# Kernel tuning notes

Hardware: AMD Instinct MI355X
Metric: run time of the kernel (lower is better)

Reference implementation:

```python
import jax, jax.numpy as jnp
import numpy as np
import math

H = 4            # cross_attn_heads
SPARSE_RATIO = 0.6
B, N, C = 128, 196, 768


def setup_inputs() -> dict:
    key = jax.random.key(0)
    ks = jax.random.split(key, 10)
    xav = (6.0 / (C + C)) ** 0.5  # xavier_uniform bound for square Linear
    inp = {
        "RGB_cash": jax.random.normal(ks[0], (B, N, C), jnp.float32),
        "NI_cash": jax.random.normal(ks[1], (B, N, C), jnp.float32),
        "TI_cash": jax.random.normal(ks[2], (B, N, C), jnp.float32),
        "RGB_global": jax.random.normal(ks[3], (B, C), jnp.float32),
        "NI_global": jax.random.normal(ks[4], (B, C), jnp.float32),
        "TI_global": jax.random.normal(ks[5], (B, C), jnp.float32),
        # 9 CrossModalAttention modules, stacked: q_proj / k_proj weights (out,in) and biases
        "q_w": jax.random.uniform(ks[6], (9, C, C), jnp.float32, -xav, xav),
        "q_b": jnp.zeros((9, C), jnp.float32),
        "k_w": jax.random.uniform(ks[7], (9, C, C), jnp.float32, -xav, xav),
        "k_b": jnp.zeros((9, C), jnp.float32),
        # 3 TokenSparse modal_weights, init torch.ones(3); small noise for non-degenerate softmax
        "modal_w": jnp.ones((3, 3), jnp.float32) + 0.01 * jax.random.normal(ks[8], (3, 3), jnp.float32),
    }
    return inp


def _cos_sim(patches, g):
    # patches (B,N,C), g (B,C) -> (B,N); F.normalize eps=1e-12
    pn = patches / jnp.maximum(jnp.linalg.norm(patches, axis=-1, keepdims=True), 1e-12)
    gn = g / jnp.maximum(jnp.linalg.norm(g, axis=-1, keepdims=True), 1e-12)
    return jnp.einsum("bnc,bc->bn", pn, gn)


def _cross_attn(patches, g, cos, qw, qb, kw, kb):
    # CrossModalAttention.forward: Q from global (1 token), K from patches, softmax over N
    b, n, c = patches.shape
    d = c // H
    q = (g @ qw.T + qb).reshape(b, H, d)              # (B,H,D)
    k = (patches @ kw.T + kb).reshape(b, n, H, d)     # (B,N,H,D)
    attn = jnp.einsum("bhd,bnhd->bhn", q, k) * (d ** -0.5)
    attn = jax.nn.softmax(attn, axis=-1)              # (B,H,N)
    return (attn * cos[:, None, :]).mean(axis=1)      # (B,N)


def _minmax(s):
    smin = s.min(axis=-1, keepdims=True)
    smax = s.max(axis=-1, keepdims=True)
    return (s - smin) / (smax - smin + 1e-8)


def _token_sparse(tokens, s_im, s_m2, s_m3, mw):
    b, n, c = tokens.shape
    w = jax.nn.softmax(mw)
    score = w[0] * _minmax(s_im) + w[1] * _minmax(s_m2) + w[2] * _minmax(s_m3)
    num_keep = max(1, math.ceil(n * SPARSE_RATIO))
    _, idx = jax.lax.top_k(score, num_keep)           # == descending sort, first num_keep
    mask = jnp.zeros((b, n), score.dtype).at[jnp.arange(b)[:, None], idx].set(1.0)
    return tokens * mask[..., None], mask


def reference(RGB_cash, NI_cash, TI_cash, RGB_global, NI_global, TI_global,
              q_w, q_b, k_w, k_b, modal_w):
    toks = [RGB_cash, NI_cash, TI_cash]
    glbs = [RGB_global, NI_global, TI_global]
    # module order: rgb_self, rgb_x_nir, rgb_x_tir, nir_self, nir_x_rgb, nir_x_tir,
    #               tir_self, tir_x_rgb, tir_x_nir
    order = [(0, 0), (0, 1), (0, 2), (1, 1), (1, 0), (1, 2), (2, 2), (2, 0), (2, 1)]
    scores = []
    for i, (pi, gi) in enumerate(order):
        cos = _cos_sim(toks[pi], glbs[gi])
        scores.append(_cross_attn(toks[pi], glbs[gi], cos, q_w[i], q_b[i], k_w[i], k_b[i]))
    out_rgb, m_rgb = _token_sparse(RGB_cash, scores[0], scores[1], scores[2], modal_w[0])
    out_nir, m_nir = _token_sparse(NI_cash, scores[3], scores[4], scores[5], modal_w[1])
    out_tir, m_tir = _token_sparse(TI_cash, scores[6], scores[7], scores[8], modal_w[2])
    return (out_rgb, out_nir, out_tir, m_rgb, m_nir, m_tir)
```

## Files before the change

### kernel.cpp

```cpp
#include <hip/hip_runtime.h>
#include <math.h>

#define BB   128
#define NN   196
#define CC   768
#define HH   4
#define DD   192
#define TOK_PER   19267584
#define NROWS_ALL 75264
#define F4_ALL    14450688
#define NUM_KEEP  118

#define OFF_QPART 0
#define SZ_QPART  (2*9*128*768)
#define OFF_VV    (OFF_QPART + SZ_QPART)
#define SZ_VV     (9*128*4*768)
#define OFF_BIAS  (OFF_VV + SZ_VV)
#define SZ_BIAS   (9*128*4)
#define OFF_GN    (OFF_BIAS + SZ_BIAS)
#define SZ_GN     (3*128*768)
#define OFF_LOG   (OFF_GN + SZ_GN)
#define SZ_LOG    (9*128*4*196)
#define OFF_COS   (OFF_LOG + SZ_LOG)

__device__ __forceinline__ float4 f4fma(float s, float4 b, float4 a) {
  a.x = fmaf(s, b.x, a.x); a.y = fmaf(s, b.y, a.y);
  a.z = fmaf(s, b.z, a.z); a.w = fmaf(s, b.w, a.w);
  return a;
}

__global__ __launch_bounds__(256) void k_gnorm(const float* __restrict__ g0,
                                               const float* __restrict__ g1,
                                               const float* __restrict__ g2,
                                               float* __restrict__ gn) {
  int wid = (blockIdx.x * 256 + threadIdx.x) >> 6;
  int lane = threadIdx.x & 63;
  if (wid >= 384) return;
  int t = wid >> 7, b = wid & 127;
  const float* src = (t == 0) ? g0 : ((t == 1) ? g1 : g2);
  const float4* s4 = (const float4*)(src + (size_t)b * CC);
  float4 v0 = s4[lane], v1 = s4[lane + 64], v2 = s4[lane + 128];
  float ss = v0.x*v0.x + v0.y*v0.y + v0.z*v0.z + v0.w*v0.w
           + v1.x*v1.x + v1.y*v1.y + v1.z*v1.z + v1.w*v1.w
           + v2.x*v2.x + v2.y*v2.y + v2.z*v2.z + v2.w*v2.w;
  #pragma unroll
  for (int off = 32; off; off >>= 1) ss += __shfl_xor(ss, off);
  float inv = 1.0f / fmaxf(sqrtf(ss), 1e-12f);
  float4* d4 = (float4*)(gn + ((size_t)t * 128 + b) * CC);
  v0.x *= inv; v0.y *= inv; v0.z *= inv; v0.w *= inv;
  v1.x *= inv; v1.y *= inv; v1.z *= inv; v1.w *= inv;
  v2.x *= inv; v2.y *= inv; v2.z *= inv; v2.w *= inv;
  d4[lane] = v0; d4[lane + 64] = v1; d4[lane + 128] = v2;
}

__global__ __launch_bounds__(256) void k_qproj(const float* __restrict__ g0,
                                               const float* __restrict__ g1,
                                               const float* __restrict__ g2,
                                               const float* __restrict__ qw,
                                               float* __restrict__ qpart) {
  __shared__ __align__(16) float AsT[32 * 68];
  __shared__ __align__(16) float WsT[32 * 68];
  const int gtab[9] = {0, 1, 2, 1, 0, 2, 2, 0, 1};
  int i = blockIdx.y, z = blockIdx.z;
  int mt = blockIdx.x & 1, nt = blockIdx.x >> 1;
  int tid = threadIdx.x, tx = tid & 15, ty = tid >> 4;
  int gi = gtab[i];
  const float4* A4 = (const float4*)((gi == 0) ? g0 : ((gi == 1) ? g1 : g2));
  const float4* W4 = (const float4*)(qw + (size_t)i * CC * CC);
  float4 acc0 = {0,0,0,0}, acc1 = {0,0,0,0}, acc2 = {0,0,0,0}, acc3 = {0,0,0,0};
  int arow = mt * 64, wrow = nt * 64;
  int kb4 = z * 96;
  for (int kk = 0; kk < 12; kk++) {
    #pragma unroll
    for (int f = tid; f < 512; f += 256) {
      int r = f >> 3, k4 = f & 7;
      float4 va = A4[(size_t)(arow + r) * 192 + kb4 + kk * 8 + k4];
      float4 vw = W4[(size_t)(wrow + r) * 192 + kb4 + kk * 8 + k4];
      int kq = 4 * k4;
      AsT[(kq+0)*68 + r] = va.x; AsT[(kq+1)*68 + r] = va.y;
      AsT[(kq+2)*68 + r] = va.z; AsT[(kq+3)*68 + r] = va.w;
      WsT[(kq+0)*68 + r] = vw.x; WsT[(kq+1)*68 + r] = vw.y;
      WsT[(kq+2)*68 + r] = vw.z; WsT[(kq+3)*68 + r] = vw.w;
    }
    __syncthreads();
    #pragma unroll
    for (int k = 0; k < 32; k++) {
      float4 a = *(const float4*)&AsT[k * 68 + 4 * ty];
      float4 w = *(const float4*)&WsT[k * 68 + 4 * tx];
      acc0 = f4fma(a.x, w, acc0); acc1 = f4fma(a.y, w, acc1);
      acc2 = f4fma(a.z, w, acc2); acc3 = f4fma(a.w, w, acc3);
    }
    __syncthreads();
  }
  float* dst = qpart + (size_t)(z * 9 + i) * 128 * CC;
  int col = wrow + 4 * tx;
  int row = arow + 4 * ty;
  *(float4*)&dst[(size_t)(row + 0) * CC + col] = acc0;
  *(float4*)&dst[(size_t)(row + 1) * CC + col] = acc1;
  *(float4*)&dst[(size_t)(row + 2) * CC + col] = acc2;
  *(float4*)&dst[(size_t)(row + 3) * CC + col] = acc3;
}

__global__ __launch_bounds__(256) void k_vvproj(const float* __restrict__ qpart,
                                                const float* __restrict__ qb,
                                                const float* __restrict__ kw,
                                                float* __restrict__ vvout) {
  __shared__ __align__(16) float AsT[32 * 68];
  __shared__ __align__(16) float Bs[32 * 68];
  int ih = blockIdx.y; int i = ih >> 2, h = ih & 3;
  int mt = blockIdx.x & 1, nt = blockIdx.x >> 1;
  int tid = threadIdx.x, tx = tid & 15, ty = tid >> 4;
  const float4* qp0 = (const float4*)qpart + (size_t)i * 128 * 192;
  const float4* qp1 = (const float4*)qpart + (size_t)(9 + i) * 128 * 192;
  const float4* qb4 = (const float4*)qb + (size_t)i * 192;
  const float4* B4  = (const float4*)(kw + (size_t)i * CC * CC);
  float4 acc0 = {0,0,0,0}, acc1 = {0,0,0,0}, acc2 = {0,0,0,0}, acc3 = {0,0,0,0};
  int arow = mt * 64;
  int bcol4 = nt * 16;
  for (int kk = 0; kk < 6; kk++) {
    #pragma unroll
    for (int f = tid; f < 512; f += 256) {
      int r = f >> 3, k4 = f & 7;
      int colf4 = h * 48 + kk * 8 + k4;
      float4 va = qp0[(size_t)(arow + r) * 192 + colf4];
      float4 vb = qp1[(size_t)(arow + r) * 192 + colf4];
      float4 vq = qb4[colf4];
      va.x += vb.x + vq.x; va.y += vb.y + vq.y;
      va.z += vb.z + vq.z; va.w += vb.w + vq.w;
      int kq = 4 * k4;
      AsT[(kq+0)*68 + r] = va.x; AsT[(kq+1)*68 + r] = va.y;
      AsT[(kq+2)*68 + r] = va.z; AsT[(kq+3)*68 + r] = va.w;
      int rk = f >> 4, c4 = f & 15;
      float4 vB = B4[(size_t)(h * DD + kk * 32 + rk) * 192 + bcol4 + c4];
      *(float4*)&Bs[rk * 68 + 4 * c4] = vB;
    }
    __syncthreads();
    #pragma unroll
    for (int k = 0; k < 32; k++) {
      float4 a = *(const float4*)&AsT[k * 68 + 4 * ty];
      float4 bb = *(const float4*)&Bs[k * 68 + 4 * tx];
      acc0 = f4fma(a.x, bb, acc0); acc1 = f4fma(a.y, bb, acc1);
      acc2 = f4fma(a.z, bb, acc2); acc3 = f4fma(a.w, bb, acc3);
    }
    __syncthreads();
  }
  int col = nt * 64 + 4 * tx;
  int b0 = arow + 4 * ty;
  *(float4*)&vvout[((size_t)(i * 128 + b0 + 0) * 4 + h) * CC + col] = acc0;
  *(float4*)&vvout[((size_t)(i * 128 + b0 + 1) * 4 + h) * CC + col] = acc1;
  *(float4*)&vvout[((size_t)(i * 128 + b0 + 2) * 4 + h) * CC + col] = acc2;
  *(float4*)&vvout[((size_t)(i * 128 + b0 + 3) * 4 + h) * CC + col] = acc3;
}

__global__ __launch_bounds__(128) void k_bias(const float* __restrict__ qpart,
                                              const float* __restrict__ qb,
                                              const float* __restrict__ kb,
                                              float* __restrict__ bias) {
  int ih = blockIdx.x; int i = ih >> 2, h = ih & 3;
  int b = threadIdx.x;
  const float* q0  = qpart + ((size_t)i * 128 + b) * CC + h * DD;
  const float* q1  = qpart + ((size_t)(9 + i) * 128 + b) * CC + h * DD;
  const float* qbb = qb + (size_t)i * CC + h * DD;
  const float* kbb = kb + (size_t)i * CC + h * DD;
  float s = 0.f;
  for (int j = 0; j < DD; j++) s = fmaf(q0[j] + q1[j] + qbb[j], kbb[j], s);
  bias[((size_t)i * 128 + b) * 4 + h] = s;
}

__global__ __launch_bounds__(128) void k_dots(const float* __restrict__ rgb,
                                              const float* __restrict__ ni,
                                              const float* __restrict__ ti,
                                              const float* __restrict__ vv,
                                              const float* __restrict__ gn,
                                              const float* __restrict__ bias,
                                              float* __restrict__ logits,
                                              float* __restrict__ cosm) {
  __shared__ __align__(16) float V[15 * 768];
  int bid = blockIdx.x;
  int t = bid >> 8;
  int rem = bid & 255;
  int b = rem >> 1, half = rem & 1;
  const float* toks = (t == 0) ? rgb : ((t == 1) ? ni : ti);
  float4* V4 = (float4*)V;
  for (int f = threadIdx.x; f < 15 * 192; f += 128) {
    int v = f / 192, c4 = f - v * 192;
    const float4* src;
    if (v < 12) {
      int k = v >> 2, h = v & 3;
      src = (const float4*)(vv + (((size_t)(3 * t + k) * 128 + b) * 4 + h) * CC);
    } else {
      src = (const float4*)(gn + ((size_t)(v - 12) * 128 + b) * CC);
    }
    V4[f] = src[c4];
  }
  __syncthreads();
  int tid = threadIdx.x;
  if (tid >= 98) return;
  int n = half * 98 + tid;
  const float4* P4 = (const float4*)(toks + ((size_t)b * NN + n) * CC);
  float acc[16];
  #pragma unroll
  for (int v = 0; v < 16; v++) acc[v] = 0.f;
  #pragma unroll 2
  for (int c4 = 0; c4 < 192; c4++) {
    float4 p = P4[c4];
    #pragma unroll
    for (int v = 0; v < 15; v++) {
      float4 q = V4[v * 192 + c4];
      acc[v] += p.x * q.x + p.y * q.y + p.z * q.z + p.w * q.w;
    }
    acc[15] += p.x * p.x + p.y * p.y + p.z * p.z + p.w * p.w;
  }
  float invp = 1.0f / fmaxf(sqrtf(acc[15]), 1e-12f);
  const float scale = 0.07216878364870322f;
  const int GI[3][3] = {{0, 1, 2}, {1, 0, 2}, {2, 0, 1}};
  #pragma unroll
  for (int k = 0; k < 3; k++) {
    int i = 3 * t + k;
    #pragma unroll
    for (int h = 0; h < 4; h++) {
      float bv = bias[((size_t)i * 128 + b) * 4 + h];
      logits[(((size_t)i * 128 + b) * 4 + h) * NN + n] = (acc[k * 4 + h] + bv) * scale;
    }
    cosm[((size_t)i * 128 + b) * NN + n] = acc[12 + GI[t][k]] * invp;
  }
}

__device__ __forceinline__ float bred_sum(float v, float* red) {
  #pragma unroll
  for (int off = 32; off; off >>= 1) v += __shfl_xor(v, off);
  int tid = threadIdx.x;
  if ((tid & 63) == 0) red[tid >> 6] = v;
  __syncthreads();
  v = (red[0] + red[1]) + (red[2] + red[3]);
  __syncthreads();
  return v;
}
__device__ __forceinline__ float bred_max(float v, float* red) {
  #pragma unroll
  for (int off = 32; off; off >>= 1) v = fmaxf(v, __shfl_xor(v, off));
  int tid = threadIdx.x;
  if ((tid & 63) == 0) red[tid >> 6] = v;
  __syncthreads();
  v = fmaxf(fmaxf(red[0], red[1]), fmaxf(red[2], red[3]));
  __syncthreads();
  return v;
}
__device__ __forceinline__ float bred_min(float v, float* red) {
  #pragma unroll
  for (int off = 32; off; off >>= 1) v = fminf(v, __shfl_xor(v, off));
  int tid = threadIdx.x;
  if ((tid & 63) == 0) red[tid >> 6] = v;
  __syncthreads();
  v = fminf(fminf(red[0], red[1]), fminf(red[2], red[3]));
  __syncthreads();
  return v;
}

__global__ __launch_bounds__(256) void k_score(const float* __restrict__ logits,
                                               const float* __restrict__ cosm,
                                               const float* __restrict__ modal_w,
                                               float* __restrict__ outmask) {
  __shared__ float red[4];
  __shared__ float sfinal[196];
  int b = blockIdx.x, m = blockIdx.y;
  int tid = threadIdx.x;
  bool act = tid < NN;
  float w0 = modal_w[m * 3 + 0], w1 = modal_w[m * 3 + 1], w2 = modal_w[m * 3 + 2];
  float wm = fmaxf(w0, fmaxf(w1, w2));
  float e0 = expf(w0 - wm), e1 = expf(w1 - wm), e2 = expf(w2 - wm);
  float esum = e0 + e1 + e2;
  float wk[3] = {e0 / esum, e1 / esum, e2 / esum};
  float finalv = 0.f;
  for (int k = 0; k < 3; k++) {
    int i = 3 * m + k;
    float asum = 0.f;
    for (int h = 0; h < 4; h++) {
      float v = act ? logits[(((size_t)i * 128 + b) * 4 + h) * NN + tid] : -3.4e38f;
      float mx = bred_max(v, red);
      float e = act ? expf(v - mx) : 0.f;
      float s = bred_sum(e, red);
      asum += e / s;
    }
    float c = act ? cosm[((size_t)i * 128 + b) * NN + tid] : 0.f;
    float sc = c * asum * 0.25f;
    float mn = bred_min(act ? sc : 3.4e38f, red);
    float mx = bred_max(act ? sc : -3.4e38f, red);
    finalv += wk[k] * (sc - mn) / (mx - mn + 1e-8f);
  }
  if (act) sfinal[tid] = finalv;
  __syncthreads();
  if (act) {
    int cnt = 0;
    for (int j = 0; j < NN; j++) {
      float fj = sfinal[j];
      cnt += (fj > finalv) || (fj == finalv && j < tid);
    }
    outmask[((size_t)m * 128 + b) * NN + tid] = (cnt < NUM_KEEP) ? 1.0f : 0.0f;
  }
}

__global__ __launch_bounds__(256) void k_write(const float* __restrict__ rgb,
                                               const float* __restrict__ ni,
                                               const float* __restrict__ ti,
                                               const float* __restrict__ maskbuf,
                                               float* __restrict__ out) {
  int idx = blockIdx.x * 256 + threadIdx.x;
  int r = idx / 192;
  int c4 = idx - r * 192;
  int m = r / 25088;
  int rb = r - m * 25088;
  float mv = maskbuf[r];
  const float* src = (m == 0) ? rgb : ((m == 1) ? ni : ti);
  float4 o = {0.f, 0.f, 0.f, 0.f};
  if (mv != 0.0f) o = ((const float4*)src)[(size_t)rb * 192 + c4];
  ((float4*)out)[idx] = o;
}

extern "C" void kernel_launch(void* const* d_in, const int* in_sizes, int n_in,
                              void* d_out, int out_size, void* d_ws, size_t ws_size,
                              hipStream_t stream) {
  const float* rgb = (const float*)d_in[0];
  const float* ni  = (const float*)d_in[1];
  const float* ti  = (const float*)d_in[2];
  const float* g0  = (const float*)d_in[3];
  const float* g1  = (const float*)d_in[4];
  const float* g2  = (const float*)d_in[5];
  const float* qw  = (const float*)d_in[6];
  const float* qb  = (const float*)d_in[7];
  const float* kw  = (const float*)d_in[8];
  const float* kb  = (const float*)d_in[9];
  const float* mw  = (const float*)d_in[10];

  float* ws    = (float*)d_ws;
  float* qpart = ws + OFF_QPART;
  float* vv    = ws + OFF_VV;
  float* bias  = ws + OFF_BIAS;
  float* gn    = ws + OFF_GN;
  float* logits= ws + OFF_LOG;
  float* cosm  = ws + OFF_COS;
  float* outf  = (float*)d_out;
  float* maskb = outf + (size_t)3 * TOK_PER;

  k_gnorm<<<96, 256, 0, stream>>>(g0, g1, g2, gn);
  k_qproj<<<dim3(24, 9, 2), 256, 0, stream>>>(g0, g1, g2, qw, qpart);
  k_vvproj<<<dim3(24, 36), 256, 0, stream>>>(qpart, qb, kw, vv);
  k_bias<<<36, 128, 0, stream>>>(qpart, qb, kb, bias);
  k_dots<<<768, 128, 0, stream>>>(rgb, ni, ti, vv, gn, bias, logits, cosm);
  k_score<<<dim3(128, 3), 256, 0, stream>>>(logits, cosm, mw, maskb);
  k_write<<<F4_ALL / 256, 256, 0, stream>>>(rgb, ni, ti, maskb, outf);
}
```

Baseline: 583.2 us.

## Restructure dot kernel to row-per-wave with register-held vectors and packed scores

```diff
diff --git a/kernel.cpp b/kernel.cpp
--- a/kernel.cpp
+++ b/kernel.cpp
@@ -10,6 +10,7 @@
 #define NROWS_ALL 75264
 #define F4_ALL    14450688
 #define NUM_KEEP  118
+#define SCALE_D   0.07216878364870322f
 
 #define OFF_QPART 0
 #define SZ_QPART  (2*9*128*768)
@@ -19,14 +20,16 @@
 #define SZ_BIAS   (9*128*4)
 #define OFF_GN    (OFF_BIAS + SZ_BIAS)
 #define SZ_GN     (3*128*768)
-#define OFF_LOG   (OFF_GN + SZ_GN)
-#define SZ_LOG    (9*128*4*196)
-#define OFF_COS   (OFF_LOG + SZ_LOG)
+#define OFF_SC    (OFF_GN + SZ_GN)
+#define SZ_SC     (3*128*196*16)
 
 __device__ __forceinline__ float4 f4fma(float s, float4 b, float4 a) {
   a.x = fmaf(s, b.x, a.x); a.y = fmaf(s, b.y, a.y);
   a.z = fmaf(s, b.z, a.z); a.w = fmaf(s, b.w, a.w);
   return a;
+}
+__device__ __forceinline__ float f4dot(float4 p, float4 q) {
+  return p.x*q.x + p.y*q.y + p.z*q.z + p.w*q.w;
 }
 
 __global__ __launch_bounds__(256) void k_gnorm(const float* __restrict__ g0,
@@ -40,9 +43,7 @@
   const float* src = (t == 0) ? g0 : ((t == 1) ? g1 : g2);
   const float4* s4 = (const float4*)(src + (size_t)b * CC);
   float4 v0 = s4[lane], v1 = s4[lane + 64], v2 = s4[lane + 128];
-  float ss = v0.x*v0.x + v0.y*v0.y + v0.z*v0.z + v0.w*v0.w
-           + v1.x*v1.x + v1.y*v1.y + v1.z*v1.z + v1.w*v1.w
-           + v2.x*v2.x + v2.y*v2.y + v2.z*v2.z + v2.w*v2.w;
+  float ss = f4dot(v0,v0) + f4dot(v1,v1) + f4dot(v2,v2);
   #pragma unroll
   for (int off = 32; off; off >>= 1) ss += __shfl_xor(ss, off);
   float inv = 1.0f / fmaxf(sqrtf(ss), 1e-12f);
@@ -167,62 +168,100 @@
   bias[((size_t)i * 128 + b) * 4 + h] = s;
 }
 
-__global__ __launch_bounds__(128) void k_dots(const float* __restrict__ rgb,
-                                              const float* __restrict__ ni,
-                                              const float* __restrict__ ti,
-                                              const float* __restrict__ vv,
-                                              const float* __restrict__ gn,
-                                              const float* __restrict__ bias,
-                                              float* __restrict__ logits,
-                                              float* __restrict__ cosm) {
-  __shared__ __align__(16) float V[15 * 768];
+__global__ __launch_bounds__(256, 2) void k_dots2(const float* __restrict__ rgb,
+                                                  const float* __restrict__ ni,
+                                                  const float* __restrict__ ti,
+                                                  const float* __restrict__ vv,
+                                                  const float* __restrict__ gn,
+                                                  const float* __restrict__ bias,
+                                                  float* __restrict__ sc) {
+  __shared__ float red[4][64 * 17];
   int bid = blockIdx.x;
   int t = bid >> 8;
   int rem = bid & 255;
   int b = rem >> 1, half = rem & 1;
+  int tid = threadIdx.x;
+  int w = tid >> 6, lane = tid & 63;
   const float* toks = (t == 0) ? rgb : ((t == 1) ? ni : ti);
-  float4* V4 = (float4*)V;
-  for (int f = threadIdx.x; f < 15 * 192; f += 128) {
-    int v = f / 192, c4 = f - v * 192;
-    const float4* src;
-    if (v < 12) {
-      int k = v >> 2, h = v & 3;
-      src = (const float4*)(vv + (((size_t)(3 * t + k) * 128 + b) * 4 + h) * CC);
-    } else {
-      src = (const float4*)(gn + ((size_t)(v - 12) * 128 + b) * CC);
-    }
-    V4[f] = src[c4];
-  }
-  __syncthreads();
-  int tid = threadIdx.x;
-  if (tid >= 98) return;
-  int n = half * 98 + tid;
-  const float4* P4 = (const float4*)(toks + ((size_t)b * NN + n) * CC);
-  float acc[16];
-  #pragma unroll
-  for (int v = 0; v < 16; v++) acc[v] = 0.f;
-  #pragma unroll 2
-  for (int c4 = 0; c4 < 192; c4++) {
-    float4 p = P4[c4];
+  int gi0, gi1, gi2;
+  if (t == 0)      { gi0 = 0; gi1 = 1; gi2 = 2; }
+  else if (t == 1) { gi0 = 1; gi1 = 0; gi2 = 2; }
+  else             { gi0 = 2; gi1 = 0; gi2 = 1; }
+
+  float4 V[45];
+  #pragma unroll
+  for (int k = 0; k < 3; k++) {
+    #pragma unroll
+    for (int h = 0; h < 4; h++) {
+      const float4* src = (const float4*)(vv + (((size_t)(3*t + k) * 128 + b) * 4 + h) * CC);
+      int v = k * 4 + h;
+      V[3*v + 0] = src[lane];
+      V[3*v + 1] = src[lane + 64];
+      V[3*v + 2] = src[lane + 128];
+    }
+  }
+  {
+    int gidx0 = gi0, gidx1 = gi1, gidx2 = gi2;
+    const float4* s0 = (const float4*)(gn + ((size_t)gidx0 * 128 + b) * CC);
+    const float4* s1 = (const float4*)(gn + ((size_t)gidx1 * 128 + b) * CC);
+    const float4* s2 = (const float4*)(gn + ((size_t)gidx2 * 128 + b) * CC);
+    V[36] = s0[lane]; V[37] = s0[lane + 64]; V[38] = s0[lane + 128];
+    V[39] = s1[lane]; V[40] = s1[lane + 64]; V[41] = s1[lane + 128];
+    V[42] = s2[lane]; V[43] = s2[lane + 64]; V[44] = s2[lane + 128];
+  }
+
+  int a_id = lane & 15;
+  float bias_r = 0.f;
+  if (a_id < 12)
+    bias_r = bias[((size_t)(3*t + (a_id >> 2)) * 128 + b) * 4 + (a_id & 3)];
+
+  float* myred = red[w];
+  int s_grp = lane >> 4;
+  int n0 = half * 98;
+
+  const float4* pr0 = (const float4*)(toks + ((size_t)b * NN + n0 + w) * CC);
+  float4 pc0 = pr0[lane], pc1 = pr0[lane + 64], pc2 = pr0[lane + 128];
+
+  for (int it = 0; it < 25; it++) {
+    int row_local = it * 4 + w;
+    if (row_local >= 98) break;
+
+    float a[16];
     #pragma unroll
     for (int v = 0; v < 15; v++) {
-      float4 q = V4[v * 192 + c4];
-      acc[v] += p.x * q.x + p.y * q.y + p.z * q.z + p.w * q.w;
-    }
-    acc[15] += p.x * p.x + p.y * p.y + p.z * p.z + p.w * p.w;
-  }
-  float invp = 1.0f / fmaxf(sqrtf(acc[15]), 1e-12f);
-  const float scale = 0.07216878364870322f;
-  const int GI[3][3] = {{0, 1, 2}, {1, 0, 2}, {2, 0, 1}};
-  #pragma unroll
-  for (int k = 0; k < 3; k++) {
-    int i = 3 * t + k;
-    #pragma unroll
-    for (int h = 0; h < 4; h++) {
-      float bv = bias[((size_t)i * 128 + b) * 4 + h];
-      logits[(((size_t)i * 128 + b) * 4 + h) * NN + n] = (acc[k * 4 + h] + bv) * scale;
-    }
-    cosm[((size_t)i * 128 + b) * NN + n] = acc[12 + GI[t][k]] * invp;
+      a[v] = f4dot(pc0, V[3*v]) + f4dot(pc1, V[3*v + 1]) + f4dot(pc2, V[3*v + 2]);
+    }
+    a[15] = f4dot(pc0, pc0) + f4dot(pc1, pc1) + f4dot(pc2, pc2);
+
+    int rl_next = row_local + 4;
+    float4 pn0, pn1, pn2;
+    if (rl_next < 98) {
+      const float4* pr = (const float4*)(toks + ((size_t)b * NN + n0 + rl_next) * CC);
+      pn0 = pr[lane]; pn1 = pr[lane + 64]; pn2 = pr[lane + 128];
+    }
+
+    #pragma unroll
+    for (int v = 0; v < 16; v++) myred[lane * 17 + v] = a[v];
+    __builtin_amdgcn_s_waitcnt(0);
+    float part = 0.f;
+    #pragma unroll
+    for (int i = 0; i < 16; i++)
+      part += myred[(s_grp * 16 + i) * 17 + a_id];
+    part += __shfl_xor(part, 16, 64);
+    part += __shfl_xor(part, 32, 64);
+
+    float s15  = __shfl(part, 15, 64);
+    float invp = 1.0f / fmaxf(sqrtf(s15), 1e-12f);
+    float res;
+    if (a_id < 12)      res = (part + bias_r) * SCALE_D;
+    else if (a_id < 15) res = part * invp;
+    else                res = invp;
+
+    if (lane < 16) {
+      float* scrow = sc + (((size_t)t * 128 + b) * 196 + (n0 + row_local)) * 16;
+      scrow[lane] = res;
+    }
+    pc0 = pn0; pc1 = pn1; pc2 = pn2;
   }
 }
 
@@ -257,8 +296,7 @@
   return v;
 }
 
-__global__ __launch_bounds__(256) void k_score(const float* __restrict__ logits,
-                                               const float* __restrict__ cosm,
+__global__ __launch_bounds__(256) void k_score(const float* __restrict__ sc,
                                                const float* __restrict__ modal_w,
                                                float* __restrict__ outmask) {
   __shared__ float red[4];
@@ -266,6 +304,7 @@
   int b = blockIdx.x, m = blockIdx.y;
   int tid = threadIdx.x;
   bool act = tid < NN;
+  const float* row = sc + (((size_t)m * 128 + b) * 196 + (act ? tid : 0)) * 16;
   float w0 = modal_w[m * 3 + 0], w1 = modal_w[m * 3 + 1], w2 = modal_w[m * 3 + 2];
   float wm = fmaxf(w0, fmaxf(w1, w2));
   float e0 = expf(w0 - wm), e1 = expf(w1 - wm), e2 = expf(w2 - wm);
@@ -273,20 +312,19 @@
   float wk[3] = {e0 / esum, e1 / esum, e2 / esum};
   float finalv = 0.f;
   for (int k = 0; k < 3; k++) {
-    int i = 3 * m + k;
     float asum = 0.f;
     for (int h = 0; h < 4; h++) {
-      float v = act ? logits[(((size_t)i * 128 + b) * 4 + h) * NN + tid] : -3.4e38f;
+      float v = act ? row[k * 4 + h] : -3.4e38f;
       float mx = bred_max(v, red);
       float e = act ? expf(v - mx) : 0.f;
       float s = bred_sum(e, red);
       asum += e / s;
     }
-    float c = act ? cosm[((size_t)i * 128 + b) * NN + tid] : 0.f;
-    float sc = c * asum * 0.25f;
-    float mn = bred_min(act ? sc : 3.4e38f, red);
-    float mx = bred_max(act ? sc : -3.4e38f, red);
-    finalv += wk[k] * (sc - mn) / (mx - mn + 1e-8f);
+    float c = act ? row[12 + k] : 0.f;
+    float scv = c * asum * 0.25f;
+    float mn = bred_min(act ? scv : 3.4e38f, red);
+    float mx = bred_max(act ? scv : -3.4e38f, red);
+    finalv += wk[k] * (scv - mn) / (mx - mn + 1e-8f);
   }
   if (act) sfinal[tid] = finalv;
   __syncthreads();
@@ -337,8 +375,7 @@
   float* vv    = ws + OFF_VV;
   float* bias  = ws + OFF_BIAS;
   float* gn    = ws + OFF_GN;
-  float* logits= ws + OFF_LOG;
-  float* cosm  = ws + OFF_COS;
+  float* sc    = ws + OFF_SC;
   float* outf  = (float*)d_out;
   float* maskb = outf + (size_t)3 * TOK_PER;
 
@@ -346,7 +383,7 @@
   k_qproj<<<dim3(24, 9, 2), 256, 0, stream>>>(g0, g1, g2, qw, qpart);
   k_vvproj<<<dim3(24, 36), 256, 0, stream>>>(qpart, qb, kw, vv);
   k_bias<<<36, 128, 0, stream>>>(qpart, qb, kb, bias);
-  k_dots<<<768, 128, 0, stream>>>(rgb, ni, ti, vv, gn, bias, logits, cosm);
-  k_score<<<dim3(128, 3), 256, 0, stream>>>(logits, cosm, mw, maskb);
+  k_dots2<<<768, 256, 0, stream>>>(rgb, ni, ti, vv, gn, bias, sc);
+  k_score<<<dim3(128, 3), 256, 0, stream>>>(sc, mw, maskb);
   k_write<<<F4_ALL / 256, 256, 0, stream>>>(rgb, ni, ti, maskb, outf);
 }
```

New measurement: 569.0 us. 2.4% less time.
